# Performance work log

Hardware: AMD Instinct MI355X
Metric: run time of the kernel (lower is better)

## Reference

```python
import jax, jax.numpy as jnp
import numpy as np

B, S, E = 2, 2048, 1024
H, D = 16, 64


def setup_inputs() -> dict:
    key = jax.random.key(0)
    ks = jax.random.split(key, 9)
    s_in = 1.0 / np.sqrt(E)
    s_out = 1.0 / np.sqrt(H * D)
    return {
        "x": jax.random.normal(ks[0], (B, S, E), dtype=jnp.float32),
        "W_q": jax.random.uniform(ks[1], (H, E, D), jnp.float32, -s_in, s_in),
        "b_q": jax.random.uniform(ks[2], (H, D), jnp.float32, -s_in, s_in),
        "W_k": jax.random.uniform(ks[3], (H, E, D), jnp.float32, -s_in, s_in),
        "b_k": jax.random.uniform(ks[4], (H, D), jnp.float32, -s_in, s_in),
        "W_v": jax.random.uniform(ks[5], (H, E, D), jnp.float32, -s_in, s_in),
        "b_v": jax.random.uniform(ks[6], (H, D), jnp.float32, -s_in, s_in),
        "W_o": jax.random.uniform(ks[7], (H * D, E), jnp.float32, -s_out, s_out),
        "b_o": jax.random.uniform(ks[8], (E,), jnp.float32, -s_out, s_out),
    }


def reference(x, W_q, b_q, W_k, b_k, W_v, b_v, W_o, b_o):
    # batched per-head projections: [B,S,E] x [H,E,D] -> [B,H,S,D]
    q = jnp.einsum("bse,hed->bhsd", x, W_q) + b_q[None, :, None, :]
    k = jnp.einsum("bse,hed->bhsd", x, W_k) + b_k[None, :, None, :]
    v = jnp.einsum("bse,hed->bhsd", x, W_v) + b_v[None, :, None, :]
    scale = 1.0 / jnp.sqrt(jnp.asarray(D, dtype=x.dtype))
    score = jnp.einsum("bhsd,bhtd->bhst", q, k) * scale  # [B,H,S,S]
    causal = jnp.tril(jnp.ones((S, S), dtype=bool))
    score = jnp.where(causal[None, None], score, -jnp.inf)
    w = jax.nn.softmax(score, axis=-1)
    o = jnp.einsum("bhst,bhtd->bhsd", w, v)  # [B,H,S,D]
    # concat heads along last dim (head-major order matches torch.cat)
    o = o.transpose(0, 2, 1, 3).reshape(B, S, H * D)
    # dropout is identity in eval mode
    return o @ W_o + b_o
```

## Files before the change

### kernel.cpp

```cpp
#include <hip/hip_runtime.h>


typedef __attribute__((ext_vector_type(8)))  __bf16 bf16x8;
typedef __attribute__((ext_vector_type(4)))  __bf16 bf16x4;
typedef __attribute__((ext_vector_type(2)))  __bf16 bf16x2;
typedef __attribute__((ext_vector_type(4)))  float  f32x4;
typedef __attribute__((ext_vector_type(16))) float  f32x16;
typedef __attribute__((ext_vector_type(2)))  unsigned int u32x2;
typedef __attribute__((ext_vector_type(4)))  unsigned int u32x4;

#define LOG2E 1.4426950408889634f
#define SM_SC (0.125f * LOG2E)
#define MBIAS (32.0f * SM_SC)

static __device__ __forceinline__ void gl2lds16(const void* g, void* l) {
    __builtin_amdgcn_global_load_lds(
        (__attribute__((address_space(1))) void*)(void*)g,
        (__attribute__((address_space(3))) void*)l, 16, 0, 0);
}

static __device__ __forceinline__ unsigned pku(float a, float b) {
    bf16x2 t = { (__bf16)a, (__bf16)b };
    return __builtin_bit_cast(unsigned, t);
}

__global__ void __launch_bounds__(256)
prep_all_kern(const float* __restrict__ x, const float* __restrict__ Wq,
              const float* __restrict__ Wk, const float* __restrict__ Wv,
              const float* __restrict__ bq, const float* __restrict__ bk,
              const float* __restrict__ bv, const float* __restrict__ Wo,
              __bf16* __restrict__ xb, __bf16* __restrict__ wt,
              float* __restrict__ bias, __bf16* __restrict__ wto) {
    __shared__ float T[64][65];
    const int t = threadIdx.x;
    const int bx = blockIdx.x;
    if (bx < 4096) {
        int i = (bx * 256 + t) * 4;
        f32x4 v = *(const f32x4*)(x + i);
        bf16x4 o = { (__bf16)v[0], (__bf16)v[1], (__bf16)v[2], (__bf16)v[3] };
        *(bf16x4*)(xb + i) = o;
    } else if (bx < 4864) {
        const int blk = bx - 4096;
        const int kt = blk & 15, ph = blk >> 4;
        const int h = ph & 15, p = ph >> 4;
        const float* W  = (p == 0) ? Wq : (p == 1) ? Wk : Wv;
        const float* bb = (p == 0) ? bq : (p == 1) ? bk : bv;
        #pragma unroll
        for (int i = 0; i < 4; ++i) {
            int flat = i * 1024 + t * 4;
            int kr = flat >> 6, d4 = flat & 63;
            f32x4 v = *(const f32x4*)(W + (h << 16) + ((kt * 64 + kr) << 6) + d4);
            T[kr][d4] = v[0]; T[kr][d4 + 1] = v[1]; T[kr][d4 + 2] = v[2]; T[kr][d4 + 3] = v[3];
        }
        __syncthreads();
        const int d = t >> 2, kq = (t & 3) << 4;
        bf16x8 o0, o1;
        #pragma unroll
        for (int j = 0; j < 8; ++j) o0[j] = (__bf16)T[kq + j][d];
        #pragma unroll
        for (int j = 0; j < 8; ++j) o1[j] = (__bf16)T[kq + 8 + j][d];
        __bf16* dst = wt + (((size_t)(p * 1024 + h * 64 + d)) << 10) + kt * 64 + kq;
        *(bf16x8*)dst = o0;
        *(bf16x8*)(dst + 8) = o1;
        if (kt == 0 && t < 64) bias[p * 1024 + h * 64 + t] = bb[h * 64 + t];
    } else {
        const int blk = bx - 4864;
        const int nt = blk & 15, ktile = blk >> 4;
        #pragma unroll
        for (int i = 0; i < 4; ++i) {
            int flat = i * 1024 + t * 4;
            int kr = flat >> 6, n4 = flat & 63;
            f32x4 v = *(const f32x4*)(Wo + ((size_t)(ktile * 64 + kr) << 10) + nt * 64 + n4);
            T[kr][n4] = v[0]; T[kr][n4 + 1] = v[1]; T[kr][n4 + 2] = v[2]; T[kr][n4 + 3] = v[3];
        }
        __syncthreads();
        const int n = t >> 2, kq = (t & 3) << 4;
        bf16x8 o0, o1;
        #pragma unroll
        for (int j = 0; j < 8; ++j) o0[j] = (__bf16)T[kq + j][n];
        #pragma unroll
        for (int j = 0; j < 8; ++j) o1[j] = (__bf16)T[kq + 8 + j][n];
        __bf16* dst = wto + (((size_t)(nt * 64 + n)) << 10) + ktile * 64 + kq;
        *(bf16x8*)dst = o0;
        *(bf16x8*)(dst + 8) = o1;
    }
}

template <int EPI>
__global__ void __launch_bounds__(256, 3)
gemm_bt(const __bf16* __restrict__ A, const __bf16* __restrict__ Bt,
        const float* __restrict__ bias,
        __bf16* __restrict__ outq, __bf16* __restrict__ outk, __bf16* __restrict__ outv,
        float* __restrict__ outf)
{
    __shared__ __align__(16) __bf16 As[128 * 64];
    __shared__ __align__(16) __bf16 Bs[128 * 64];
    const int tid = threadIdx.x;
    const int wid = tid >> 6, lane = tid & 63;
    const int r = lane & 15, g = lane >> 4;
    const int m0 = blockIdx.y << 7, n0 = blockIdx.x << 7;
    const int wr = wid >> 1, wc = wid & 1;
    f32x4 acc[4][4] = {};
    for (int k0 = 0; k0 < 1024; k0 += 64) {
        #pragma unroll
        for (int c = 0; c < 4; ++c) {
            int cq = (c * 4 + wid) * 64 + lane;
            int row = cq >> 3, ci = cq & 7;
            int cis = ci ^ (row & 7);
            gl2lds16(A  + (((size_t)(m0 + row)) << 10) + k0 + cis * 8, As + (c * 4 + wid) * 512);
            gl2lds16(Bt + (((size_t)(n0 + row)) << 10) + k0 + cis * 8, Bs + (c * 4 + wid) * 512);
        }
        __syncthreads();
        bf16x8 af[2][4], bfr[2][4];
        #pragma unroll
        for (int kh = 0; kh < 2; ++kh)
            #pragma unroll
            for (int i = 0; i < 4; ++i) {
                int pc = ((kh * 4 + g) ^ (r & 7)) * 8;
                af[kh][i]  = *(const bf16x8*)&As[(wr * 64 + i * 16 + r) * 64 + pc];
                bfr[kh][i] = *(const bf16x8*)&Bs[(wc * 64 + i * 16 + r) * 64 + pc];
            }
        #pragma unroll
        for (int kh = 0; kh < 2; ++kh)
            #pragma unroll
            for (int mi = 0; mi < 4; ++mi)
                #pragma unroll
                for (int ni = 0; ni < 4; ++ni)
                    acc[mi][ni] = __builtin_amdgcn_mfma_f32_16x16x32_bf16(
                        af[kh][mi], bfr[kh][ni], acc[mi][ni], 0, 0, 0);
        __syncthreads();
    }
    if (EPI == 0) {
        #pragma unroll
        for (int ni = 0; ni < 4; ++ni) {
            int n = n0 + wc * 64 + ni * 16 + r;
            float bv = bias[n];
            int p = n >> 10, rem = n & 1023, h = rem >> 6, d = rem & 63;
            #pragma unroll
            for (int mi = 0; mi < 4; ++mi) {
                int mb = m0 + wr * 64 + mi * 16 + g * 4;
                int b = mb >> 11, s = mb & 2047;
                f32x4 v = acc[mi][ni];
                if (p < 2) {
                    __bf16* dst = (p == 0) ? outq : outk;
                    size_t base = (((size_t)(b * 16 + h)) * 2048 + s) * 64 + d;
                    #pragma unroll
                    for (int j = 0; j < 4; ++j)
                        dst[base + (size_t)j * 64] = (__bf16)(v[j] + bv);
                } else {
                    bf16x4 pk = { (__bf16)(v[0] + bv), (__bf16)(v[1] + bv),
                                  (__bf16)(v[2] + bv), (__bf16)(v[3] + bv) };
                    *(bf16x4*)&outv[(((size_t)(b * 16 + h)) * 64 + d) * 2048 + s] = pk;
                }
            }
        }
    } else {
        #pragma unroll
        for (int ni = 0; ni < 4; ++ni) {
            int n = n0 + wc * 64 + ni * 16 + r;
            float bv = bias[n];
            #pragma unroll
            for (int mi = 0; mi < 4; ++mi) {
                int mb = m0 + wr * 64 + mi * 16 + g * 4;
                f32x4 v = acc[mi][ni];
                #pragma unroll
                for (int j = 0; j < 4; ++j)
                    outf[((size_t)(mb + j) << 10) + n] = v[j] + bv;
            }
        }
    }
}

__global__ void __launch_bounds__(256, 3)
attn_kern(const __bf16* __restrict__ q, const __bf16* __restrict__ k,
          const __bf16* __restrict__ vT, __bf16* __restrict__ pO0,
          __bf16* __restrict__ pO1, __bf16* __restrict__ pO2,
          __bf16* __restrict__ pO3, float* __restrict__ ml)
{
    __shared__ __align__(16) __bf16 Ks [2][64][72];
    __shared__ __align__(16) __bf16 VsT[2][64][72];
    const int tid = threadIdx.x, lane = tid & 63, w = tid >> 6;
    const int r31 = lane & 31, hi = lane >> 5;
    const int bid = blockIdx.x;
    const int rnk = bid >> 5, bh = bid & 31;
    const int j = 15 - (rnk >> 2), kvq = rnk & 3;
    const int b = bh >> 4, h = bh & 15;
    const __bf16* qh  = q  + ((size_t)bh << 17);
    const __bf16* khp = k  + ((size_t)bh << 17);
    const __bf16* vhp = vT + ((size_t)bh << 17);
    __bf16* pO = (kvq == 0) ? pO0 : (kvq == 1) ? pO1 : (kvq == 2) ? pO2 : pO3;
    const int srow = tid >> 3, sci = tid & 7;

    const int qb0 = j << 7;
    const int wrow0 = qb0 + w * 32;
    const int mg = wrow0 + r31;
    const int c2 = 2 * (j + 1);
    const int base = c2 >> 2, rem = c2 & 3;
    const int len = base + (kvq < rem ? 1 : 0);
    const int tbeg = kvq * base + min(kvq, rem);
    const int tend = tbeg + len;

    f32x16 oacc[2] = {};
    f32x16 lacc = {};

    if (len > 0) {
        bf16x8 qf[4];
        #pragma unroll
        for (int kk = 0; kk < 4; ++kk)
            qf[kk] = *(const bf16x8*)&qh[(size_t)mg * 64 + kk * 16 + hi * 8];
        bf16x8 onesf;
        #pragma unroll
        for (int jj = 0; jj < 8; ++jj) onesf[jj] = (__bf16)1.0f;

        #pragma unroll
        for (int it = 0; it < 2; ++it) {
            int row = srow + it * 32;
            *(bf16x8*)&Ks [0][row][sci * 8] = *(const bf16x8*)&khp[(size_t)(tbeg * 64 + row) * 64 + sci * 8];
            *(bf16x8*)&VsT[0][row][sci * 8] = *(const bf16x8*)&vhp[(size_t)row * 2048 + tbeg * 64 + sci * 8];
        }
        __syncthreads();

        for (int t = tbeg; t < tend; ++t) {
            const int cur = (t - tbeg) & 1, nxt = cur ^ 1;
            const int n0 = t << 6;
            const bool pre = (t + 1 < tend);
            bf16x8 nk[2], nv[2];
            if (pre) {
                int n1 = n0 + 64;
                #pragma unroll
                for (int it = 0; it < 2; ++it) {
                    int row = srow + it * 32;
                    nk[it] = *(const bf16x8*)&khp[(size_t)(n1 + row) * 64 + sci * 8];
                    nv[it] = *(const bf16x8*)&vhp[(size_t)row * 2048 + n1 + sci * 8];
                }
            }
            if (n0 <= wrow0 + 31) {
                f32x16 sacc[2] = {};
                #pragma unroll
                for (int kk = 0; kk < 4; ++kk) {
                    bf16x8 kf0 = *(const bf16x8*)&Ks[cur][r31]     [kk * 16 + hi * 8];
                    bf16x8 kf1 = *(const bf16x8*)&Ks[cur][32 + r31][kk * 16 + hi * 8];
                    sacc[0] = __builtin_amdgcn_mfma_f32_32x32x16_bf16(kf0, qf[kk], sacc[0], 0, 0, 0);
                    sacc[1] = __builtin_amdgcn_mfma_f32_32x32x16_bf16(kf1, qf[kk], sacc[1], 0, 0, 0);
                }
                if (n0 + 63 > wrow0) {
                    #pragma unroll
                    for (int nf = 0; nf < 2; ++nf)
                        #pragma unroll
                        for (int i = 0; i < 16; ++i) {
                            int n = n0 + nf * 32 + (i & 3) + 8 * (i >> 2) + 4 * hi;
                            if (n > mg) sacc[nf][i] = -3.0e38f;
                        }
                }
                #pragma unroll
                for (int nf = 0; nf < 2; ++nf)
                    #pragma unroll
                    for (int i = 0; i < 16; ++i)
                        sacc[nf][i] = exp2f(fmaf(sacc[nf][i], SM_SC, -MBIAS));
                #pragma unroll
                for (int nf = 0; nf < 2; ++nf) {
                    unsigned pk[8];
                    #pragma unroll
                    for (int jj = 0; jj < 8; ++jj)
                        pk[jj] = pku(sacc[nf][2 * jj], sacc[nf][2 * jj + 1]);
#if __has_builtin(__builtin_amdgcn_permlane32_swap)
                    u32x2 s02 = __builtin_amdgcn_permlane32_swap(pk[0], pk[2], false, false);
                    u32x2 s13 = __builtin_amdgcn_permlane32_swap(pk[1], pk[3], false, false);
                    u32x2 s46 = __builtin_amdgcn_permlane32_swap(pk[4], pk[6], false, false);
                    u32x2 s57 = __builtin_amdgcn_permlane32_swap(pk[5], pk[7], false, false);
                    u32x4 fw0 = { s02[0], s13[0], s02[1], s13[1] };
                    u32x4 fw1 = { s46[0], s57[0], s46[1], s57[1] };
#else
                    unsigned rxa = __shfl_xor(hi ? pk[0] : pk[2], 32);
                    unsigned rxb = __shfl_xor(hi ? pk[1] : pk[3], 32);
                    unsigned rxc = __shfl_xor(hi ? pk[4] : pk[6], 32);
                    unsigned rxd = __shfl_xor(hi ? pk[5] : pk[7], 32);
                    u32x4 fw0 = { hi ? rxa : pk[0], hi ? rxb : pk[1],
                                  hi ? pk[2] : rxa, hi ? pk[3] : rxb };
                    u32x4 fw1 = { hi ? rxc : pk[4], hi ? rxd : pk[5],
                                  hi ? pk[6] : rxc, hi ? pk[7] : rxd };
#endif
                    bf16x8 pf0 = __builtin_bit_cast(bf16x8, fw0);
                    bf16x8 pf1 = __builtin_bit_cast(bf16x8, fw1);
                    #pragma unroll
                    for (int kl = 0; kl < 2; ++kl) {
                        const bf16x8 pf = kl ? pf1 : pf0;
                        const int kk = nf * 2 + kl;
                        bf16x8 af0 = *(const bf16x8*)&VsT[cur][r31]     [kk * 16 + hi * 8];
                        bf16x8 af1 = *(const bf16x8*)&VsT[cur][32 + r31][kk * 16 + hi * 8];
                        oacc[0] = __builtin_amdgcn_mfma_f32_32x32x16_bf16(af0, pf, oacc[0], 0, 0, 0);
                        oacc[1] = __builtin_amdgcn_mfma_f32_32x32x16_bf16(af1, pf, oacc[1], 0, 0, 0);
                        lacc    = __builtin_amdgcn_mfma_f32_32x32x16_bf16(onesf, pf, lacc, 0, 0, 0);
                    }
                }
            }
            if (pre) {
                #pragma unroll
                for (int it = 0; it < 2; ++it) {
                    int row = srow + it * 32;
                    *(bf16x8*)&Ks [nxt][row][sci * 8] = nk[it];
                    *(bf16x8*)&VsT[nxt][row][sci * 8] = nv[it];
                }
            }
            __syncthreads();
        }
    }
    #pragma unroll
    for (int df = 0; df < 2; ++df)
        #pragma unroll
        for (int td = 0; td < 8; ++td) {
            bf16x2 pr = { (__bf16)oacc[df][2 * td], (__bf16)oacc[df][2 * td + 1] };
            int d = df * 32 + 8 * (td >> 1) + 4 * hi + 2 * (td & 1);
            *(bf16x2*)&pO[((size_t)(b * 2048 + mg) << 10) + h * 64 + d] = pr;
        }
    if (hi == 0)
        ml[((size_t)(kvq * 32 + bh) << 11) + mg] = lacc[0];
}

__global__ void merge_kern(const __bf16* __restrict__ pO0, const __bf16* __restrict__ pO2,
                           const __bf16* __restrict__ pO3, const float* __restrict__ ml,
                           __bf16* __restrict__ ob)
{
    int i = blockIdx.x * 256 + threadIdx.x;
    int m = i >> 7, rem = i & 127, h = rem >> 3, d8 = (rem & 7) * 8;
    int bh = (m >> 11) * 16 + h, sr = m & 2047;
    size_t i0 = ((size_t)bh << 11) + sr;
    float lsum = ml[i0] + ml[65536 + i0] + ml[131072 + i0] + ml[196608 + i0];
    float inv = 1.0f / lsum;
    size_t off = (size_t)m * 1024 + h * 64 + d8;
    bf16x8 a0 = *(const bf16x8*)(pO0 + off);
    bf16x8 a1 = *(const bf16x8*)(ob + off);
    bf16x8 a2 = *(const bf16x8*)(pO2 + off);
    bf16x8 a3 = *(const bf16x8*)(pO3 + off);
    bf16x8 r;
    #pragma unroll
    for (int j = 0; j < 8; ++j)
        r[j] = (__bf16)(((float)a0[j] + (float)a1[j] + (float)a2[j] + (float)a3[j]) * inv);
    *(bf16x8*)(ob + off) = r;
}

extern "C" void kernel_launch(void* const* d_in, const int* in_sizes, int n_in,
                              void* d_out, int out_size, void* d_ws, size_t ws_size,
                              hipStream_t stream) {
    const float* x  = (const float*)d_in[0];
    const float* Wq = (const float*)d_in[1];
    const float* bq = (const float*)d_in[2];
    const float* Wk = (const float*)d_in[3];
    const float* bk = (const float*)d_in[4];
    const float* Wv = (const float*)d_in[5];
    const float* bv = (const float*)d_in[6];
    const float* Wo = (const float*)d_in[7];
    const float* bo = (const float*)d_in[8];
    float* out = (float*)d_out;
    char* ws = (char*)d_ws;
    __bf16* xb    = (__bf16*)(ws + 0);
    __bf16* wtqkv = (__bf16*)(ws + 8388608);
    __bf16* wot   = (__bf16*)(ws + 14680064);
    float*  biasq = (float*) (ws + 16777216);
    __bf16* qb    = (__bf16*)(ws + 16793600);
    __bf16* kb    = (__bf16*)(ws + 25182208);
    __bf16* vtb   = (__bf16*)(ws + 33570816);
    __bf16* ob    = (__bf16*)(ws + 41959424);
    __bf16* pO0   = xb;
    __bf16* pO2   = (__bf16*)d_out;
    __bf16* pO3   = (__bf16*)d_out + 4194304;
    float*  mlbuf = (float*)(ws + 8388608);

    prep_all_kern<<<5120, 256, 0, stream>>>(x, Wq, Wk, Wv, bq, bk, bv, Wo,
                                            xb, wtqkv, biasq, wot);
    gemm_bt<0><<<dim3(24, 32), 256, 0, stream>>>(xb, wtqkv, biasq, qb, kb, vtb, nullptr);
    attn_kern<<<2048, 256, 0, stream>>>(qb, kb, vtb, pO0, ob, pO2, pO3, mlbuf);
    merge_kern<<<2048, 256, 0, stream>>>(pO0, pO2, pO3, mlbuf, ob);
    gemm_bt<1><<<dim3(8, 32), 256, 0, stream>>>(ob, wot, bo, nullptr, nullptr, nullptr, out);
}
```

Baseline: 110.4 us.

## Fuse split-KV partial merge into output projection GEMM prologue

Adds a gemm_o kernel that reads the four split-KV partial outputs plus the softmax sums, normalizes and merges them while staging the A tile into LDS, then runs the output projection. The separate merge kernel launch and its write and re-read of the merged bf16 buffer go away. Partials move into workspace when it is large enough, so the output buffer is no longer used as scratch. In exchange, every N-block column recomputes the merge (8x redundant reads of the partials), and A is loaded synchronously instead of through global_load_lds.

```diff
diff --git a/kernel.cpp b/kernel.cpp
--- a/kernel.cpp
+++ b/kernel.cpp
@@ -167,6 +167,79 @@
                 for (int j = 0; j < 4; ++j)
                     outf[((size_t)(mb + j) << 10) + n] = v[j] + bv;
             }
+        }
+    }
+}
+
+__global__ void __launch_bounds__(256, 3)
+gemm_o(const __bf16* __restrict__ pO0, const __bf16* __restrict__ pO1,
+       const __bf16* __restrict__ pO2, const __bf16* __restrict__ pO3,
+       const float* __restrict__ ml, const __bf16* __restrict__ Bt,
+       const float* __restrict__ bias, float* __restrict__ outf)
+{
+    __shared__ __align__(16) __bf16 As[128 * 64];
+    __shared__ __align__(16) __bf16 Bs[128 * 64];
+    const int tid = threadIdx.x;
+    const int wid = tid >> 6, lane = tid & 63;
+    const int r = lane & 15, g = lane >> 4;
+    const int m0 = blockIdx.y << 7, n0 = blockIdx.x << 7;
+    const int wr = wid >> 1, wc = wid & 1;
+    f32x4 acc[4][4] = {};
+    for (int k0 = 0; k0 < 1024; k0 += 64) {
+        const int h = k0 >> 6;
+        #pragma unroll
+        for (int c = 0; c < 4; ++c) {
+            int cq = (c * 4 + wid) * 64 + lane;
+            int row = cq >> 3, ci = cq & 7;
+            int cis = ci ^ (row & 7);
+            int m = m0 + row, b = m >> 11, sr = m & 2047;
+            size_t i0 = ((size_t)(b * 16 + h) << 11) + sr;
+            float lsum = ml[i0] + ml[65536 + i0] + ml[131072 + i0] + ml[196608 + i0];
+            float inv = 1.0f / lsum;
+            size_t off = ((size_t)m << 10) + k0 + cis * 8;
+            bf16x8 a0 = *(const bf16x8*)(pO0 + off);
+            bf16x8 a1 = *(const bf16x8*)(pO1 + off);
+            bf16x8 a2 = *(const bf16x8*)(pO2 + off);
+            bf16x8 a3 = *(const bf16x8*)(pO3 + off);
+            bf16x8 mv;
+            #pragma unroll
+            for (int jj = 0; jj < 8; ++jj)
+                mv[jj] = (__bf16)(((float)a0[jj] + (float)a1[jj] +
+                                   (float)a2[jj] + (float)a3[jj]) * inv);
+            *(bf16x8*)&As[cq * 8] = mv;
+            gl2lds16(Bt + (((size_t)(n0 + row)) << 10) + k0 + cis * 8, Bs + (c * 4 + wid) * 512);
+        }
+        __syncthreads();
+        bf16x8 af[2][4], bfr[2][4];
+        #pragma unroll
+        for (int kh = 0; kh < 2; ++kh)
+            #pragma unroll
+            for (int i = 0; i < 4; ++i) {
+                int pc = ((kh * 4 + g) ^ (r & 7)) * 8;
+                af[kh][i]  = *(const bf16x8*)&As[(wr * 64 + i * 16 + r) * 64 + pc];
+                bfr[kh][i] = *(const bf16x8*)&Bs[(wc * 64 + i * 16 + r) * 64 + pc];
+            }
+        #pragma unroll
+        for (int kh = 0; kh < 2; ++kh)
+            #pragma unroll
+            for (int mi = 0; mi < 4; ++mi)
+                #pragma unroll
+                for (int ni = 0; ni < 4; ++ni)
+                    acc[mi][ni] = __builtin_amdgcn_mfma_f32_16x16x32_bf16(
+                        af[kh][mi], bfr[kh][ni], acc[mi][ni], 0, 0, 0);
+        __syncthreads();
+    }
+    #pragma unroll
+    for (int ni = 0; ni < 4; ++ni) {
+        int n = n0 + wc * 64 + ni * 16 + r;
+        float bv = bias[n];
+        #pragma unroll
+        for (int mi = 0; mi < 4; ++mi) {
+            int mb = m0 + wr * 64 + mi * 16 + g * 4;
+            f32x4 v = acc[mi][ni];
+            #pragma unroll
+            for (int j = 0; j < 4; ++j)
+                outf[((size_t)(mb + j) << 10) + n] = v[j] + bv;
         }
     }
 }
@@ -362,14 +435,20 @@
     __bf16* vtb   = (__bf16*)(ws + 33570816);
     __bf16* ob    = (__bf16*)(ws + 41959424);
     __bf16* pO0   = xb;
-    __bf16* pO2   = (__bf16*)d_out;
-    __bf16* pO3   = (__bf16*)d_out + 4194304;
     float*  mlbuf = (float*)(ws + 8388608);
+
+    const bool fused = (ws_size >= 67125248ULL);
+    __bf16* pO2 = fused ? (__bf16*)(ws + 50348032) : (__bf16*)d_out;
+    __bf16* pO3 = fused ? (__bf16*)(ws + 58736640) : ((__bf16*)d_out + 4194304);
 
     prep_all_kern<<<5120, 256, 0, stream>>>(x, Wq, Wk, Wv, bq, bk, bv, Wo,
                                             xb, wtqkv, biasq, wot);
     gemm_bt<0><<<dim3(24, 32), 256, 0, stream>>>(xb, wtqkv, biasq, qb, kb, vtb, nullptr);
     attn_kern<<<2048, 256, 0, stream>>>(qb, kb, vtb, pO0, ob, pO2, pO3, mlbuf);
-    merge_kern<<<2048, 256, 0, stream>>>(pO0, pO2, pO3, mlbuf, ob);
-    gemm_bt<1><<<dim3(8, 32), 256, 0, stream>>>(ob, wot, bo, nullptr, nullptr, nullptr, out);
-}
+    if (fused) {
+        gemm_o<<<dim3(8, 32), 256, 0, stream>>>(pO0, ob, pO2, pO3, mlbuf, wot, bo, out);
+    } else {
+        merge_kern<<<2048, 256, 0, stream>>>(pO0, pO2, pO3, mlbuf, ob);
+        gemm_bt<1><<<dim3(8, 32), 256, 0, stream>>>(ob, wot, bo, nullptr, nullptr, nullptr, out);
+    }
+}
```

Result: slower. 200.4 us (+81.5%).
